# Kernel optimization log

Hardware: AMD Instinct MI355X
Metric: run time of the kernel (lower is better)

## Reference

```python
import jax, jax.numpy as jnp
import numpy as np

B, T, C, H, S = 4, 2048, 1024, 16, 64
LN_EPS = 1e-5
WKV_EPS = 1e-6
K_CLAMP = 30.0


def _ln(x, g, b):
    m = jnp.mean(x, axis=-1, keepdims=True)
    v = jnp.var(x, axis=-1, keepdims=True)
    return (x - m) * jax.lax.rsqrt(v + LN_EPS) * g + b


def _wkv(k, v, time_decay, time_first):
    # k, v: [B,T,H,S]; recurrence in fp32 over time
    decay = jnp.exp(-jnp.exp(time_decay.astype(jnp.float32)))  # [H,S]
    tf = jnp.exp(time_first.astype(jnp.float32))               # [H,S]
    kt = jnp.moveaxis(k, 1, 0).astype(jnp.float32)  # [T,B,H,S]
    vt = jnp.moveaxis(v, 1, 0).astype(jnp.float32)
    # t == 0 special case: state seeded with time_first factor
    w0 = jnp.exp(jnp.minimum(kt[0], K_CLAMP))
    num0 = tf * w0 * vt[0]
    den0 = tf * w0

    def step(carry, xs):
        num, den = carry
        kk, vv = xs
        w = jnp.exp(jnp.minimum(kk, K_CLAMP))
        num = decay * num + w * vv
        den = decay * den + w
        return (num, den), num / (den + WKV_EPS)

    (_, _), rest = jax.lax.scan(step, (num0, den0), (kt[1:], vt[1:]))
    out = jnp.concatenate([(num0 / (den0 + WKV_EPS))[None], rest], axis=0)  # [T,B,H,S]
    return jnp.moveaxis(out, 0, 1)  # [B,T,H,S]


def setup_inputs() -> dict:
    key = jax.random.key(0)
    ks = jax.random.split(key, 8)
    sc = 1.0 / np.sqrt(C)
    sc4 = 1.0 / np.sqrt(4 * C)
    return {
        "x": jax.random.normal(ks[0], (B, T, C), jnp.float32),
        "time_decay": jnp.full((H, S), -5.0, jnp.float32),
        "time_first": jnp.zeros((H, S), jnp.float32),
        "Wk": jax.random.normal(ks[1], (C, C), jnp.float32) * sc,
        "Wv": jax.random.normal(ks[2], (C, C), jnp.float32) * sc,
        "Wr": jax.random.normal(ks[3], (C, C), jnp.float32) * sc,
        "Wo": jax.random.normal(ks[4], (C, C), jnp.float32) * sc,
        "Wffk": jax.random.normal(ks[5], (4 * C, C), jnp.float32) * sc,
        "Wffv": jax.random.normal(ks[6], (C, 4 * C), jnp.float32) * sc4,
        "ln1_g": jnp.ones((C,), jnp.float32),
        "ln1_b": jnp.zeros((C,), jnp.float32),
        "ln2_g": jnp.ones((C,), jnp.float32),
        "ln2_b": jnp.zeros((C,), jnp.float32),
    }


def reference(x, time_decay, time_first, Wk, Wv, Wr, Wo, Wffk, Wffv, ln1_g, ln1_b, ln2_g, ln2_b):
    b, t, c = x.shape
    h, s = time_decay.shape
    xl = _ln(x, ln1_g, ln1_b)
    k = (xl @ Wk.T).reshape(b, t, h, s)
    v = (xl @ Wv.T).reshape(b, t, h, s)
    r = (xl @ Wr.T).reshape(b, t, h, s)
    wkv = _wkv(k, v, time_decay, time_first).astype(x.dtype)
    rwkv = (jax.nn.sigmoid(r) * wkv).reshape(b, t, c)
    x = x + rwkv @ Wo.T
    xl2 = _ln(x, ln2_g, ln2_b)
    ffn = (jax.nn.relu(xl2 @ Wffk.T) ** 2) @ Wffv.T
    return x + ffn
```

## Files before the change

kernel.cpp:

```cpp
#include <hip/hip_runtime.h>
#include <cstdint>
#include <cstddef>

#define TT 2048
#define CC 1024
#define HH 16
#define SS 64
#define MROWS 8192
#define KVRN 3072
#define NCH 32
#define LCH 64

using short8 = __attribute__((ext_vector_type(8))) short;
using f32x4  = __attribute__((ext_vector_type(4))) float;

__device__ __forceinline__ float b2f(unsigned short u) {
  union { unsigned int i; float f; } c; c.i = ((unsigned int)u) << 16; return c.f;
}
__device__ __forceinline__ unsigned short f2b(float f) {
  union { float f; unsigned int i; } c; c.f = f;
  unsigned int r = c.i + 0x7fffu + ((c.i >> 16) & 1u);
  return (unsigned short)(r >> 16);
}

typedef const __attribute__((address_space(1))) unsigned int* gas_ptr;
typedef __attribute__((address_space(3))) unsigned int* las_ptr;
__device__ __forceinline__ void gl_lds16(const unsigned short* g, unsigned short* l) {
  __builtin_amdgcn_global_load_lds((gas_ptr)g, (las_ptr)l, 16, 0, 0);
}

__global__ __launch_bounds__(256) void cvt_ln_kernel(const float* __restrict__ Wk,
                                                     const float* __restrict__ Wv,
                                                     const float* __restrict__ Wr,
                                                     const float* __restrict__ Wo,
                                                     const float* __restrict__ Wffk,
                                                     const float* __restrict__ Wffv,
                                                     unsigned short* __restrict__ dst,
                                                     const float* __restrict__ x,
                                                     const float* __restrict__ g,
                                                     const float* __restrict__ bta,
                                                     unsigned short* __restrict__ xlo) {
  const size_t M1 = 1048576;
  const int tid = threadIdx.x;
  if (blockIdx.x < 12288) {
    size_t i = ((size_t)blockIdx.x * 256 + tid) * 4;
    const float* src; size_t off;
    if      (i <  1 * M1) { src = Wk;   off = 0;      }
    else if (i <  2 * M1) { src = Wv;   off = 1 * M1; }
    else if (i <  3 * M1) { src = Wr;   off = 2 * M1; }
    else if (i <  4 * M1) { src = Wo;   off = 3 * M1; }
    else if (i <  8 * M1) { src = Wffk; off = 4 * M1; }
    else                  { src = Wffv; off = 8 * M1; }
    float4 v = *(const float4*)(src + (i - off));
    *(ushort4*)(dst + i) = make_ushort4(f2b(v.x), f2b(v.y), f2b(v.z), f2b(v.w));
    return;
  }
  const int row = blockIdx.x - 12288;
  const float* xr = x + (size_t)row * CC;
  float4 v = *(const float4*)(xr + tid * 4);
  float s  = v.x + v.y + v.z + v.w;
  float ss = v.x * v.x + v.y * v.y + v.z * v.z + v.w * v.w;
#pragma unroll
  for (int off = 32; off > 0; off >>= 1) {
    s  += __shfl_xor(s, off, 64);
    ss += __shfl_xor(ss, off, 64);
  }
  __shared__ float ls[4], lss[4];
  if ((tid & 63) == 0) { ls[tid >> 6] = s; lss[tid >> 6] = ss; }
  __syncthreads();
  s  = ls[0] + ls[1] + ls[2] + ls[3];
  ss = lss[0] + lss[1] + lss[2] + lss[3];
  const float mean = s * (1.0f / CC);
  const float var  = ss * (1.0f / CC) - mean * mean;
  const float rstd = rsqrtf(var + 1e-5f);
  float4 gv = *(const float4*)(g + tid * 4);
  float4 bv = *(const float4*)(bta + tid * 4);
  ushort4 o = make_ushort4(f2b((v.x - mean) * rstd * gv.x + bv.x),
                           f2b((v.y - mean) * rstd * gv.y + bv.y),
                           f2b((v.z - mean) * rstd * gv.z + bv.z),
                           f2b((v.w - mean) * rstd * gv.w + bv.w));
  *(ushort4*)(xlo + (size_t)row * CC + tid * 4) = o;
}

__global__ __launch_bounds__(256) void ln_kernel(const float* __restrict__ x,
                                                 const float* __restrict__ g,
                                                 const float* __restrict__ bta,
                                                 unsigned short* __restrict__ out) {
  const int row = blockIdx.x;
  const int tid = threadIdx.x;
  const float* xr = x + (size_t)row * CC;
  float4 v = *(const float4*)(xr + tid * 4);
  float s  = v.x + v.y + v.z + v.w;
  float ss = v.x * v.x + v.y * v.y + v.z * v.z + v.w * v.w;
#pragma unroll
  for (int off = 32; off > 0; off >>= 1) {
    s  += __shfl_xor(s, off, 64);
    ss += __shfl_xor(ss, off, 64);
  }
  __shared__ float ls[4], lss[4];
  if ((tid & 63) == 0) { ls[tid >> 6] = s; lss[tid >> 6] = ss; }
  __syncthreads();
  s  = ls[0] + ls[1] + ls[2] + ls[3];
  ss = lss[0] + lss[1] + lss[2] + lss[3];
  const float mean = s * (1.0f / CC);
  const float var  = ss * (1.0f / CC) - mean * mean;
  const float rstd = rsqrtf(var + 1e-5f);
  float4 gv = *(const float4*)(g + tid * 4);
  float4 bv = *(const float4*)(bta + tid * 4);
  ushort4 o = make_ushort4(f2b((v.x - mean) * rstd * gv.x + bv.x),
                           f2b((v.y - mean) * rstd * gv.y + bv.y),
                           f2b((v.z - mean) * rstd * gv.z + bv.z),
                           f2b((v.w - mean) * rstd * gv.w + bv.w));
  *(ushort4*)(out + (size_t)row * CC + tid * 4) = o;
}

__global__ __launch_bounds__(64) void wkv_local(const unsigned short* __restrict__ kvr,
                                                const float* __restrict__ td,
                                                const float* __restrict__ tfp,
                                                float* __restrict__ scratch) {
  const int blk = blockIdx.x;
  const int bh = blk >> 5, c = blk & (NCH - 1);
  const int b = bh >> 4, h = bh & 15;
  const int s = threadIdx.x;
  const int ch = h * SS + s;
  const float e = __expf(td[ch]);
  const float d = __expf(-e);
  const float tfir = __expf(tfp[ch]);
  size_t idx = ((size_t)b * TT + (size_t)c * LCH) * KVRN + ch;
  float num = 0.f, den = 0.f;
  for (int i = 0; i < LCH; ++i) {
    float w = __expf(fminf(b2f(kvr[idx]), 30.f));
    if (c == 0 && i == 0) w *= tfir;
    float vv = b2f(kvr[idx + 1024]);
    num = d * num + w * vv;
    den = d * den + w;
    idx += KVRN;
  }
  float* o = scratch + ((size_t)bh * NCH + c) * 128;
  o[s] = num; o[64 + s] = den;
}

__global__ __launch_bounds__(64) void wkv_emit(const unsigned short* __restrict__ kvr,
                                               const float* __restrict__ td,
                                               const float* __restrict__ tfp,
                                               const float* __restrict__ scratch,
                                               unsigned short* __restrict__ rwkv) {
  const int blk = blockIdx.x;
  const int bh = blk >> 5, c = blk & (NCH - 1);
  const int b = bh >> 4, h = bh & 15;
  const int s = threadIdx.x;
  const int ch = h * SS + s;
  const float e = __expf(td[ch]);
  const float d = __expf(-e);
  const float Dc = __expf(-e * (float)LCH);
  const float tfir = __expf(tfp[ch]);
  float num = 0.f, den = 0.f;
  const float* sc = scratch + (size_t)bh * NCH * 128;
  for (int cc = 0; cc < c; ++cc) {
    num = Dc * num + sc[cc * 128 + s];
    den = Dc * den + sc[cc * 128 + 64 + s];
  }
  size_t idx = ((size_t)b * TT + (size_t)c * LCH) * KVRN + ch;
  size_t odx = ((size_t)b * TT + (size_t)c * LCH) * CC + ch;
  for (int i = 0; i < LCH; ++i) {
    float w = __expf(fminf(b2f(kvr[idx]), 30.f));
    if (c == 0 && i == 0) w *= tfir;
    float vv = b2f(kvr[idx + 1024]);
    num = d * num + w * vv;
    den = d * den + w;
    float o = num / (den + 1e-6f);
    float rr = b2f(kvr[idx + 2048]);
    float sg = 1.0f / (1.0f + __expf(-rr));
    rwkv[odx] = f2b(sg * o);
    idx += KVRN;
    odx += CC;
  }
}

template <int EP>
__global__ __launch_bounds__(256, 3) void gemm_bt(const unsigned short* __restrict__ A,
                                                  const unsigned short* __restrict__ Bw,
                                                  void* __restrict__ outv,
                                                  const float* __restrict__ res,
                                                  int N, int K) {
  __shared__ __align__(16) unsigned short As[3][128 * 32];
  __shared__ __align__(16) unsigned short Bs[3][128 * 32];
  const int tid = threadIdx.x;

  const int nbn = N >> 7;
  const int per_grp = nbn << 4;
  const int bid = blockIdx.x;
  const int grp = bid / per_grp;
  const int rem = bid - grp * per_grp;
  const int bm = (grp << 4) + (rem & 15);
  const int bn = rem >> 4;

  const int ch0 = tid, ch1 = tid + 256;
  const int r0 = ch0 >> 2, q0 = (ch0 & 3) ^ ((ch0 >> 3) & 3);
  const int r1 = ch1 >> 2, q1 = (ch1 & 3) ^ ((ch1 >> 3) & 3);
  const unsigned short* ga0 = A  + (size_t)(bm * 128 + r0) * K + q0 * 8;
  const unsigned short* ga1 = A  + (size_t)(bm * 128 + r1) * K + q1 * 8;
  const unsigned short* gb0 = Bw + (size_t)(bn * 128 + r0) * K + q0 * 8;
  const unsigned short* gb1 = Bw + (size_t)(bn * 128 + r1) * K + q1 * 8;
  const int so0 = ch0 * 8, so1 = ch1 * 8;

  const int lane = tid & 63;
  const int w    = tid >> 6;
  const int q    = lane >> 4, r16 = lane & 15;
  const int qs   = q ^ ((r16 >> 1) & 3);
  const int wrow = (w >> 1) * 64, wcol = (w & 1) * 64;

  f32x4 acc[4][4] = {};

  auto stage = [&](int b3) {
    gl_lds16(ga0, &As[b3][so0]);
    gl_lds16(ga1, &As[b3][so1]);
    gl_lds16(gb0, &Bs[b3][so0]);
    gl_lds16(gb1, &Bs[b3][so1]);
    ga0 += 32; ga1 += 32; gb0 += 32; gb1 += 32;
  };

  const int iters = K >> 5;
  stage(0);
  stage(1);

  int cb = 0, pb = 2;
  for (int i = 0; i < iters; ++i) {
    __builtin_amdgcn_s_waitcnt(0x0F74);
    __builtin_amdgcn_sched_barrier(0);
    asm volatile("s_barrier");
    __builtin_amdgcn_sched_barrier(0);
    if (i + 2 < iters) stage(pb);

    const unsigned short* Ab = &As[cb][0];
    const unsigned short* Bb = &Bs[cb][0];
    short8 af[4], bfr[4];
#pragma unroll
    for (int mi = 0; mi < 4; ++mi)
      af[mi] = *(const short8*)(Ab + ((wrow + mi * 16 + r16) * 4 + qs) * 8);
#pragma unroll
    for (int ni = 0; ni < 4; ++ni)
      bfr[ni] = *(const short8*)(Bb + ((wcol + ni * 16 + r16) * 4 + qs) * 8);
#pragma unroll
    for (int mi = 0; mi < 4; ++mi)
#pragma unroll
      for (int ni = 0; ni < 4; ++ni)
        acc[mi][ni] = __builtin_amdgcn_mfma_f32_16x16x32_bf16(af[mi], bfr[ni], acc[mi][ni], 0, 0, 0);

    cb = (cb == 2) ? 0 : cb + 1;
    pb = (pb == 2) ? 0 : pb + 1;
  }

#pragma unroll
  for (int mi = 0; mi < 4; ++mi) {
#pragma unroll
    for (int r = 0; r < 4; ++r) {
      const int grow = bm * 128 + wrow + mi * 16 + q * 4 + r;
#pragma unroll
      for (int ni = 0; ni < 4; ++ni) {
        const int gcol = bn * 128 + wcol + ni * 16 + r16;
        const size_t idx = (size_t)grow * N + gcol;
        float vv = acc[mi][ni][r];
        if (EP == 2) {
          ((float*)outv)[idx] = res[idx] + vv;
        } else {
          if (EP == 1) { vv = fmaxf(vv, 0.0f); vv = vv * vv; }
          ((unsigned short*)outv)[idx] = f2b(vv);
        }
      }
    }
  }
}

extern "C" void kernel_launch(void* const* d_in, const int* in_sizes, int n_in,
                              void* d_out, int out_size, void* d_ws, size_t ws_size,
                              hipStream_t stream) {
  const float* x    = (const float*)d_in[0];
  const float* td   = (const float*)d_in[1];
  const float* tf   = (const float*)d_in[2];
  const float* Wk   = (const float*)d_in[3];
  const float* Wv   = (const float*)d_in[4];
  const float* Wr   = (const float*)d_in[5];
  const float* Wo   = (const float*)d_in[6];
  const float* Wffk = (const float*)d_in[7];
  const float* Wffv = (const float*)d_in[8];
  const float* g1   = (const float*)d_in[9];
  const float* b1   = (const float*)d_in[10];
  const float* g2   = (const float*)d_in[11];
  const float* b2   = (const float*)d_in[12];
  float* out = (float*)d_out;

  char* ws = (char*)d_ws;
  const size_t MB = 1024ull * 1024ull;
  unsigned short* WB    = (unsigned short*)ws;
  unsigned short* WkvrB = WB;
  unsigned short* WoB   = WB + 3 * 1048576;
  unsigned short* WfkB  = WB + 4 * 1048576;
  unsigned short* WfvB  = WB + 8 * 1048576;
  unsigned short* xl    = (unsigned short*)(ws + 24 * MB);
  unsigned short* kvr   = (unsigned short*)(ws + 40 * MB);
  float*          x2    = (float*)(ws + 88 * MB);
  unsigned short* hb    = (unsigned short*)(ws + 120 * MB);
  float*          wkvS  = (float*)(ws + 184 * MB);
  unsigned short* rwkv  = xl;
  unsigned short* xl2   = kvr;

  cvt_ln_kernel<<<12288 + MROWS, 256, 0, stream>>>(Wk, Wv, Wr, Wo, Wffk, Wffv, WB,
                                                   x, g1, b1, xl);

  gemm_bt<0><<<(KVRN / 128) * (MROWS / 128), 256, 0, stream>>>(xl, WkvrB, kvr, nullptr, KVRN, 1024);

  wkv_local<<<64 * NCH, 64, 0, stream>>>(kvr, td, tf, wkvS);
  wkv_emit<<<64 * NCH, 64, 0, stream>>>(kvr, td, tf, wkvS, rwkv);

  gemm_bt<2><<<(CC / 128) * (MROWS / 128), 256, 0, stream>>>(rwkv, WoB, x2, x, 1024, 1024);

  ln_kernel<<<MROWS, 256, 0, stream>>>(x2, g2, b2, xl2);

  gemm_bt<1><<<(4096 / 128) * (MROWS / 128), 256, 0, stream>>>(xl2, WfkB, hb, nullptr, 4096, 1024);

  gemm_bt<2><<<(CC / 128) * (MROWS / 128), 256, 0, stream>>>(hb, WfvB, out, x2, 1024, 4096);
}
```

Measured before the change: 438.4 us.

## Load GEMM B operand directly into registers instead of LDS staging

The GEMM kernel stops staging the weight (B) tiles through shared memory. Each lane now loads its B fragments straight from global memory into registers, double-buffered one iteration ahead. K also becomes a template parameter so the loop trip count is a compile-time constant and can be partially unrolled. This halves LDS traffic and shared-memory footprint, and removes the B LDS reads. The cost is uncoalesced global loads for B, since each lane reads 16 bytes from a different row, plus extra register pressure and duplicated B reads across waves sharing a column.

Result: slower. 610.0 us (+39.2%).

```diff
diff --git a/kernel.cpp b/kernel.cpp
--- a/kernel.cpp
+++ b/kernel.cpp
@@ -177,14 +177,13 @@
   }
 }
 
-template <int EP>
+template <int EP, int K>
 __global__ __launch_bounds__(256, 3) void gemm_bt(const unsigned short* __restrict__ A,
                                                   const unsigned short* __restrict__ Bw,
                                                   void* __restrict__ outv,
                                                   const float* __restrict__ res,
-                                                  int N, int K) {
+                                                  int N) {
   __shared__ __align__(16) unsigned short As[3][128 * 32];
-  __shared__ __align__(16) unsigned short Bs[3][128 * 32];
   const int tid = threadIdx.x;
 
   const int nbn = N >> 7;
@@ -198,10 +197,8 @@
   const int ch0 = tid, ch1 = tid + 256;
   const int r0 = ch0 >> 2, q0 = (ch0 & 3) ^ ((ch0 >> 3) & 3);
   const int r1 = ch1 >> 2, q1 = (ch1 & 3) ^ ((ch1 >> 3) & 3);
-  const unsigned short* ga0 = A  + (size_t)(bm * 128 + r0) * K + q0 * 8;
-  const unsigned short* ga1 = A  + (size_t)(bm * 128 + r1) * K + q1 * 8;
-  const unsigned short* gb0 = Bw + (size_t)(bn * 128 + r0) * K + q0 * 8;
-  const unsigned short* gb1 = Bw + (size_t)(bn * 128 + r1) * K + q1 * 8;
+  const unsigned short* ga0 = A + (size_t)(bm * 128 + r0) * K + q0 * 8;
+  const unsigned short* ga1 = A + (size_t)(bm * 128 + r1) * K + q1 * 8;
   const int so0 = ch0 * 8, so1 = ch1 * 8;
 
   const int lane = tid & 63;
@@ -210,45 +207,68 @@
   const int qs   = q ^ ((r16 >> 1) & 3);
   const int wrow = (w >> 1) * 64, wcol = (w & 1) * 64;
 
+  const unsigned short* gbp[4];
+#pragma unroll
+  for (int ni = 0; ni < 4; ++ni)
+    gbp[ni] = Bw + (size_t)(bn * 128 + wcol + ni * 16 + r16) * K + q * 8;
+
   f32x4 acc[4][4] = {};
 
-  auto stage = [&](int b3) {
+  auto stageA = [&](int b3) {
     gl_lds16(ga0, &As[b3][so0]);
     gl_lds16(ga1, &As[b3][so1]);
-    gl_lds16(gb0, &Bs[b3][so0]);
-    gl_lds16(gb1, &Bs[b3][so1]);
-    ga0 += 32; ga1 += 32; gb0 += 32; gb1 += 32;
+    ga0 += 32; ga1 += 32;
   };
 
-  const int iters = K >> 5;
-  stage(0);
-  stage(1);
+  constexpr int ITERS = K >> 5;
+  stageA(0);
+  stageA(1);
+  short8 bcur[4], bnxt[4];
+#pragma unroll
+  for (int ni = 0; ni < 4; ++ni) { bcur[ni] = *(const short8*)gbp[ni]; gbp[ni] += 32; }
 
   int cb = 0, pb = 2;
-  for (int i = 0; i < iters; ++i) {
+#pragma unroll 2
+  for (int i = 0; i < ITERS - 1; ++i) {
+    __builtin_amdgcn_s_waitcnt(0x0F76);
+    __builtin_amdgcn_sched_barrier(0);
+    asm volatile("s_barrier");
+    __builtin_amdgcn_sched_barrier(0);
+    if (i + 2 < ITERS) stageA(pb);
+#pragma unroll
+    for (int ni = 0; ni < 4; ++ni) { bnxt[ni] = *(const short8*)gbp[ni]; gbp[ni] += 32; }
+
+    const unsigned short* Ab = &As[cb][0];
+    short8 af[4];
+#pragma unroll
+    for (int mi = 0; mi < 4; ++mi)
+      af[mi] = *(const short8*)(Ab + ((wrow + mi * 16 + r16) * 4 + qs) * 8);
+#pragma unroll
+    for (int mi = 0; mi < 4; ++mi)
+#pragma unroll
+      for (int ni = 0; ni < 4; ++ni)
+        acc[mi][ni] = __builtin_amdgcn_mfma_f32_16x16x32_bf16(af[mi], bcur[ni], acc[mi][ni], 0, 0, 0);
+
+#pragma unroll
+    for (int ni = 0; ni < 4; ++ni) bcur[ni] = bnxt[ni];
+    cb = (cb == 2) ? 0 : cb + 1;
+    pb = (pb == 2) ? 0 : pb + 1;
+  }
+  {
     __builtin_amdgcn_s_waitcnt(0x0F74);
     __builtin_amdgcn_sched_barrier(0);
     asm volatile("s_barrier");
     __builtin_amdgcn_sched_barrier(0);
-    if (i + 2 < iters) stage(pb);
-
     const unsigned short* Ab = &As[cb][0];
-    const unsigned short* Bb = &Bs[cb][0];
-    short8 af[4], bfr[4];
+    short8 af[4];
 #pragma unroll
     for (int mi = 0; mi < 4; ++mi)
       af[mi] = *(const short8*)(Ab + ((wrow + mi * 16 + r16) * 4 + qs) * 8);
 #pragma unroll
-    for (int ni = 0; ni < 4; ++ni)
-      bfr[ni] = *(const short8*)(Bb + ((wcol + ni * 16 + r16) * 4 + qs) * 8);
-#pragma unroll
     for (int mi = 0; mi < 4; ++mi)
 #pragma unroll
       for (int ni = 0; ni < 4; ++ni)
-        acc[mi][ni] = __builtin_amdgcn_mfma_f32_16x16x32_bf16(af[mi], bfr[ni], acc[mi][ni], 0, 0, 0);
-
-    cb = (cb == 2) ? 0 : cb + 1;
-    pb = (pb == 2) ? 0 : pb + 1;
+        acc[mi][ni] = __builtin_amdgcn_mfma_f32_16x16x32_bf16(af[mi], bcur[ni], acc[mi][ni], 0, 0, 0);
   }
 
 #pragma unroll
@@ -308,16 +328,16 @@
   cvt_ln_kernel<<<12288 + MROWS, 256, 0, stream>>>(Wk, Wv, Wr, Wo, Wffk, Wffv, WB,
                                                    x, g1, b1, xl);
 
-  gemm_bt<0><<<(KVRN / 128) * (MROWS / 128), 256, 0, stream>>>(xl, WkvrB, kvr, nullptr, KVRN, 1024);
+  gemm_bt<0, 1024><<<(KVRN / 128) * (MROWS / 128), 256, 0, stream>>>(xl, WkvrB, kvr, nullptr, KVRN);
 
   wkv_local<<<64 * NCH, 64, 0, stream>>>(kvr, td, tf, wkvS);
   wkv_emit<<<64 * NCH, 64, 0, stream>>>(kvr, td, tf, wkvS, rwkv);
 
-  gemm_bt<2><<<(CC / 128) * (MROWS / 128), 256, 0, stream>>>(rwkv, WoB, x2, x, 1024, 1024);
+  gemm_bt<2, 1024><<<(CC / 128) * (MROWS / 128), 256, 0, stream>>>(rwkv, WoB, x2, x, 1024);
 
   ln_kernel<<<MROWS, 256, 0, stream>>>(x2, g2, b2, xl2);
 
-  gemm_bt<1><<<(4096 / 128) * (MROWS / 128), 256, 0, stream>>>(xl2, WfkB, hb, nullptr, 4096, 1024);
-
-  gemm_bt<2><<<(CC / 128) * (MROWS / 128), 256, 0, stream>>>(hb, WfvB, out, x2, 1024, 4096);
-}
+  gemm_bt<1, 1024><<<(4096 / 128) * (MROWS / 128), 256, 0, stream>>>(xl2, WfkB, hb, nullptr, 4096);
+
+  gemm_bt<2, 4096><<<(CC / 128) * (MROWS / 128), 256, 0, stream>>>(hb, WfvB, out, x2, 1024);
+}
```
